# Kernel optimization log

Measured on AMD Instinct MI355X. Metric: run time of the kernel, lower is better.

## Reference

```python
import jax, jax.numpy as jnp
import numpy as np

NUM_PRICAPS, DIM_PRICAPS = 1152, 8
NUM_OBJCAPS, DIM_OBJCAPS = 10, 16
ROUTINGS = 3


def squash(v, axis=-1):
    norm = jnp.linalg.norm(v, axis=axis, keepdims=True)
    scale = norm ** 2 / (1.0 + norm ** 2) / (norm + 1e-8)
    return scale * v


def conv2d(x, w, b, stride):
    out = jax.lax.conv_general_dilated(
        x, w, window_strides=(stride, stride), padding='VALID',
        dimension_numbers=('NCHW', 'OIHW', 'NCHW'))
    return out + b[None, :, None, None]


def setup_inputs() -> dict:
    key = jax.random.key(0)
    ks = jax.random.split(key, 12)
    f32 = jnp.float32
    x = jax.random.uniform(ks[0], (512, 1, 28, 28), dtype=f32)
    conv1_w = jax.random.normal(ks[1], (256, 1, 9, 9), f32) / np.sqrt(1 * 81)
    conv1_b = jnp.zeros((256,), f32)
    conv2_w = jax.random.normal(ks[2], (256, 256, 9, 9), f32) / np.sqrt(256 * 81)
    conv2_b = jnp.zeros((256,), f32)
    route_w = 0.1 * jax.random.normal(ks[3], (NUM_OBJCAPS, NUM_PRICAPS, DIM_OBJCAPS, DIM_PRICAPS), f32)
    d_in = NUM_OBJCAPS * DIM_OBJCAPS  # 160
    dec1_w = jax.random.normal(ks[4], (512, d_in), f32) / np.sqrt(d_in)
    dec1_b = jnp.zeros((512,), f32)
    dec2_w = jax.random.normal(ks[5], (1024, 512), f32) / np.sqrt(512)
    dec2_b = jnp.zeros((1024,), f32)
    dec3_w = jax.random.normal(ks[6], (784, 1024), f32) / np.sqrt(1024)
    dec3_b = jnp.zeros((784,), f32)
    return {'x': x, 'conv1_w': conv1_w, 'conv1_b': conv1_b,
            'conv2_w': conv2_w, 'conv2_b': conv2_b, 'route_w': route_w,
            'dec1_w': dec1_w, 'dec1_b': dec1_b, 'dec2_w': dec2_w,
            'dec2_b': dec2_b, 'dec3_w': dec3_w, 'dec3_b': dec3_b}


def reference(x, conv1_w, conv1_b, conv2_w, conv2_b, route_w,
              dec1_w, dec1_b, dec2_w, dec2_b, dec3_w, dec3_b):
    B = x.shape[0]
    # Encoder: two convs (no activation in original), then capsulate + squash
    h = conv2d(x, conv1_w, conv1_b, 1)            # [B,256,20,20]
    h = conv2d(h, conv2_w, conv2_b, 2)            # [B,256,6,6]
    pricaps = squash(jnp.transpose(h, (0, 2, 3, 1)).reshape(B, NUM_PRICAPS, DIM_PRICAPS))
    # Votes: weight [o,i,k,d] @ incaps [b,i,d] -> [b,o,i,k]
    hat = jnp.einsum('oikd,bid->boik', route_w, pricaps)  # [B,10,1152,16]
    hat_det = jax.lax.stop_gradient(hat)
    b_log = jnp.zeros((B, NUM_OBJCAPS, NUM_PRICAPS), x.dtype)
    c = jax.nn.softmax(jnp.ones((B, NUM_OBJCAPS, NUM_PRICAPS), x.dtype), axis=1)
    outcaps = None
    for i in range(ROUTINGS):
        if i < ROUTINGS - 1:
            outcaps = squash(jnp.sum(c[:, :, :, None] * hat_det, axis=2, keepdims=True))  # [B,10,1,16]
            b_log = b_log + jnp.sum(outcaps * hat_det, axis=-1)
            c = jax.nn.softmax(b_log, axis=1)
        else:
            outcaps = squash(jnp.sum(c[:, :, :, None] * hat, axis=2, keepdims=True))
    objcaps = outcaps[:, :, 0, :]                 # [B,10,16]
    objcaps_len = jnp.linalg.norm(objcaps, axis=-1)  # [B,10]
    # Decoder: reconstruct only the max-length class capsule
    idx_max = jnp.argmax(objcaps_len, axis=1)
    y_onehot = jax.nn.one_hot(idx_max, NUM_OBJCAPS, dtype=objcaps.dtype)
    oc = (objcaps * y_onehot[:, :, None]).reshape(B, -1)  # [B,160]
    d = jax.nn.relu(oc @ dec1_w.T + dec1_b)
    d = jax.nn.relu(d @ dec2_w.T + dec2_b)
    d = jax.nn.sigmoid(d @ dec3_w.T + dec3_b)
    x_recon = jnp.clip(d.reshape(B, 1, 28, 28), 0.0, 1.0)
    return (objcaps_len, x_recon)
```

## Files before the change

### kernel.cpp

```cpp
#include <hip/hip_runtime.h>

typedef short short8 __attribute__((ext_vector_type(8)));
typedef float floatx4 __attribute__((ext_vector_type(4)));

__device__ __forceinline__ unsigned short bf16rn(float x) {
  union { float f; unsigned int u; } v; v.f = x;
  unsigned int r = v.u + 0x7fffu + ((v.u >> 16) & 1u);
  return (unsigned short)(r >> 16);
}
__device__ __forceinline__ float bf16f(unsigned short h) {
  union { unsigned int u; float f; } v; v.u = ((unsigned int)h) << 16;
  return v.f;
}
__device__ __forceinline__ void gload16(const void* g, void* l) {
  __builtin_amdgcn_global_load_lds((const __attribute__((address_space(1))) unsigned int*)g,
                                   (__attribute__((address_space(3))) unsigned int*)l, 16, 0, 0);
}
__device__ __forceinline__ unsigned swz128(int row) {
  return ((row & 1) << 6) | ((row & 2) << 4) | ((row & 4) << 2);
}

__global__ __launch_bounds__(256) void k_w2p(const float* __restrict__ w2,
                                             unsigned short* __restrict__ w2p) {
  __shared__ float sm[20736];
  const int t = threadIdx.x;
  const int co = blockIdx.x;
  for (int q = t; q < 20736; q += 256) sm[q] = w2[(size_t)co * 20736 + q];
  __syncthreads();
  const unsigned s4 = ((co & 1) << 2) | (co & 2) | ((co & 4) >> 2);
  unsigned short* base = w2p + (size_t)co * 64;
  for (int q = t; q < 5184; q += 256) {
    int kk = q >> 6, r = q & 63, cb = r >> 3, cp = r & 7;
    unsigned src = (unsigned)cp ^ s4;
    int half = src >> 2, oct = src & 3;
    const float* col = &sm[(cb * 32 + oct * 8) * 81 + kk];
    union { unsigned short u[8]; uint4 v; } pk;
#pragma unroll
    for (int j = 0; j < 8; ++j) {
      float v = col[j * 81];
      unsigned short hi = bf16rn(v);
      pk.u[j] = half ? bf16rn(v - bf16f(hi)) : hi;
    }
    *(uint4*)(base + (size_t)(kk * 8 + cb) * 16384 + cp * 8) = pk.v;
  }
}

__global__ __launch_bounds__(256) void k_conv1(const float* __restrict__ x, const float* __restrict__ w1,
                                               const float* __restrict__ b1,
                                               unsigned short* __restrict__ h1h,
                                               unsigned short* __restrict__ h1l, int b0) {
  __shared__ float xs[784];
  __shared__ float wsm[64 * 81];
  const int t = threadIdx.x;
  const int b = b0 + blockIdx.x;
  const int coq = blockIdx.y;
  for (int q = t; q < 784; q += 256) xs[q] = x[(size_t)b * 784 + q];
  for (int q = t; q < 5184; q += 256) wsm[q] = w1[coq * 5184 + q];
  __syncthreads();
  const int col = t & 63, yg = t >> 6;
  const int co = coq * 64 + col;
  const float bv = b1[co];
  unsigned short* oh = h1h + (size_t)blockIdx.x * 102400 + co;
  unsigned short* ol = h1l + (size_t)blockIdx.x * 102400 + co;
  for (int yy = 0; yy < 5; ++yy) {
    const int y = yg * 5 + yy;
    float acc[20];
#pragma unroll
    for (int i = 0; i < 20; ++i) acc[i] = bv;
    for (int ky = 0; ky < 9; ++ky) {
      float row[28];
#pragma unroll
      for (int cc = 0; cc < 28; ++cc) row[cc] = xs[(y + ky) * 28 + cc];
#pragma unroll
      for (int kx = 0; kx < 9; ++kx) {
        float wv = wsm[col * 81 + ky * 9 + kx];
#pragma unroll
        for (int xx = 0; xx < 20; ++xx) acc[xx] += row[xx + kx] * wv;
      }
    }
#pragma unroll
    for (int xx = 0; xx < 20; ++xx) {
      unsigned short hi = bf16rn(acc[xx]);
      unsigned short lo = bf16rn(acc[xx] - bf16f(hi));
      size_t p = (size_t)(y * 20 + xx) * 256;
      oh[p] = hi; ol[p] = lo;
    }
  }
}

__global__ __launch_bounds__(256) void k_conv2m(const unsigned short* __restrict__ h1h,
                                                const unsigned short* __restrict__ h1l,
                                                const unsigned short* __restrict__ w2p,
                                                float* __restrict__ part, int b0) {
  __shared__ __align__(16) char smem[40960];
  const int t = threadIdx.x;
  const int lin = blockIdx.x + 144 * blockIdx.z;
  const int xcd = lin & 7, idx = lin >> 3;
  const int zz = xcd & 3;
  const int n0 = ((xcd >> 2) * 72 + idx) * 64;
  const int kk0 = (zz == 0) ? 0 : (21 + 20 * (zz - 1));
  const int kkn = (zz == 0) ? 21 : 20;

  const int wid = t >> 6, lane = t & 63;
  const int l15 = lane & 15, l4 = lane >> 4;
  const int brow = t >> 2, bc4 = t & 3;
  size_t bsrc;
  {
    int nloc = n0 + brow;
    int bi = nloc / 36, pp = nloc - bi * 36;
    int oy = pp / 6, ox = pp - oy * 6;
    bsrc = ((size_t)((bi * 20 + 2 * oy) * 20 + 2 * ox)) * 256;
  }
  const unsigned bswz = swz128(brow);
  const unsigned bo_hi = (unsigned)(brow * 128) + (((unsigned)(bc4 * 16)) ^ bswz);
  const unsigned bo_lo = (unsigned)(brow * 128) + (((unsigned)(64 + bc4 * 16)) ^ bswz);

  floatx4 acc[4][4];
#pragma unroll
  for (int i = 0; i < 4; ++i)
#pragma unroll
    for (int j = 0; j < 4; ++j) acc[i][j] = (floatx4)0.f;

  for (int kq = 0; kq < kkn; ++kq) {
    const int kk = kk0 + kq;
    const int ky = kk / 9, kx = kk - ky * 9;
    const int koff = (ky * 20 + kx) * 256;
    for (int cb = 0; cb < 8; ++cb) {
      const unsigned short* abase = w2p + (size_t)(kk * 8 + cb) * 16384;
#pragma unroll
      for (int j = 0; j < 8; ++j) {
        const int seg = j * 4 + wid;
        gload16(abase + seg * 512 + lane * 8, smem + seg * 1024);
      }
      {
        const unsigned short* sh = h1h + bsrc + koff + cb * 32 + bc4 * 8;
        const unsigned short* sl = h1l + bsrc + koff + cb * 32 + bc4 * 8;
        uint4 vh = *(const uint4*)sh;
        uint4 vl = *(const uint4*)sl;
        *(uint4*)(smem + 32768 + bo_hi) = vh;
        *(uint4*)(smem + 32768 + bo_lo) = vl;
      }
      __syncthreads();
      short8 bh[4], blo[4];
#pragma unroll
      for (int nf = 0; nf < 4; ++nf) {
        const int br = nf * 16 + l15;
        const unsigned s = swz128(br);
        bh[nf] = *(const short8*)(smem + 32768 + br * 128 + (((unsigned)(l4 * 16)) ^ s));
        blo[nf] = *(const short8*)(smem + 32768 + br * 128 + (((unsigned)(64 + l4 * 16)) ^ s));
      }
#pragma unroll
      for (int mf = 0; mf < 4; ++mf) {
        const int ar = wid * 64 + mf * 16 + l15;
        const unsigned s = swz128(ar);
        short8 ah = *(const short8*)(smem + ar * 128 + (((unsigned)(l4 * 16)) ^ s));
        short8 al = *(const short8*)(smem + ar * 128 + (((unsigned)(64 + l4 * 16)) ^ s));
#pragma unroll
        for (int nf = 0; nf < 4; ++nf) {
          acc[mf][nf] = __builtin_amdgcn_mfma_f32_16x16x32_bf16(ah, bh[nf], acc[mf][nf], 0, 0, 0);
          acc[mf][nf] = __builtin_amdgcn_mfma_f32_16x16x32_bf16(ah, blo[nf], acc[mf][nf], 0, 0, 0);
          acc[mf][nf] = __builtin_amdgcn_mfma_f32_16x16x32_bf16(al, bh[nf], acc[mf][nf], 0, 0, 0);
        }
      }
      __syncthreads();
    }
  }
  float* po = part + (size_t)zz * 4718592;
#pragma unroll
  for (int mf = 0; mf < 4; ++mf) {
#pragma unroll
    for (int nf = 0; nf < 4; ++nf) {
      int cog = wid * 64 + mf * 16 + l4 * 4;
      int ng = b0 * 36 + n0 + nf * 16 + l15;
      *(floatx4*)&po[(size_t)ng * 256 + cog] = acc[mf][nf];
    }
  }
}

__global__ __launch_bounds__(256) void k_redsquash(const float* __restrict__ part,
                                                   const float* __restrict__ b2,
                                                   float* __restrict__ pri) {
  const int idx = blockIdx.x * 256 + threadIdx.x;
  const int n = idx >> 5, cap = idx & 31;
  const size_t o = (size_t)n * 256 + cap * 8;
  float s[8];
#pragma unroll
  for (int j = 0; j < 8; ++j) s[j] = b2[cap * 8 + j];
#pragma unroll
  for (int z = 0; z < 4; ++z) {
    const float4 a0 = *(const float4*)&part[(size_t)z * 4718592 + o];
    const float4 a1 = *(const float4*)&part[(size_t)z * 4718592 + o + 4];
    s[0] += a0.x; s[1] += a0.y; s[2] += a0.z; s[3] += a0.w;
    s[4] += a1.x; s[5] += a1.y; s[6] += a1.z; s[7] += a1.w;
  }
  float ss = 0.f;
#pragma unroll
  for (int j = 0; j < 8; ++j) ss += s[j] * s[j];
  float nn = sqrtf(ss);
  float sc = ss / (1.f + ss) / (nn + 1e-8f);
  float4 o0, o1;
  o0.x = s[0] * sc; o0.y = s[1] * sc; o0.z = s[2] * sc; o0.w = s[3] * sc;
  o1.x = s[4] * sc; o1.y = s[5] * sc; o1.z = s[6] * sc; o1.w = s[7] * sc;
  *(float4*)&pri[o] = o0;
  *(float4*)&pri[o + 4] = o1;
}

__global__ __launch_bounds__(256, 2) void k_passA(const float* __restrict__ rw, const float* __restrict__ pri,
                                                  const float* __restrict__ cbuf, float* __restrict__ spart,
                                                  int iter) {
  __shared__ __align__(16) float rw_s[16 * 516];
  __shared__ __align__(16) float p_s[16 * 516];
  __shared__ __align__(16) float c_s[1024];
  const int t = threadIdx.x;
  const int b0 = blockIdx.x * 16, i0 = blockIdx.y * 64, o = blockIdx.z;
  const float* rsrc = rw + (size_t)o * 147456 + (size_t)i0 * 128;
  for (int m = t; m < 2048; m += 256) {
    int il = m >> 5, r = m & 31, d = r >> 1, kh = (m & 1) * 4;
    float4 v = *(const float4*)&rsrc[il * 128 + d * 8 + kh];
    *(float4*)&rw_s[d * 516 + il * 8 + kh] = v;
  }
  for (int m = t; m < 2048; m += 256) {
    int bl = m >> 7, off = (m & 127) * 4;
    float4 v = *(const float4*)&pri[(size_t)(b0 + bl) * 9216 + i0 * 8 + off];
    *(float4*)&p_s[bl * 516 + off] = v;
  }
  if (iter > 0) {
    for (int m = t; m < 256; m += 256) {
      int bl = m >> 4, il4 = (m & 15) * 4;
      float4 v = *(const float4*)&cbuf[(size_t)((b0 + bl) * 10 + o) * 1152 + i0 + il4];
      *(float4*)&c_s[bl * 64 + il4] = v;
    }
  }
  __syncthreads();
  const int d = t & 15, bl = t >> 4;
  float acc = 0.f;
  for (int il = 0; il < 64; ++il) {
    float cv = (iter == 0) ? 0.1f : c_s[bl * 64 + il];
    float4 p0 = *(float4*)&p_s[bl * 516 + il * 8];
    float4 p1 = *(float4*)&p_s[bl * 516 + il * 8 + 4];
    float4 r0 = *(float4*)&rw_s[d * 516 + il * 8];
    float4 r1 = *(float4*)&rw_s[d * 516 + il * 8 + 4];
    float dt = r0.x * p0.x + r0.y * p0.y + r0.z * p0.z + r0.w * p0.w +
               r1.x * p1.x + r1.y * p1.y + r1.z * p1.z + r1.w * p1.w;
    acc += cv * dt;
  }
  spart[((size_t)blockIdx.y * 512 + (b0 + bl)) * 160 + o * 16 + d] = acc;
}

__global__ __launch_bounds__(256) void k_reduce(const float* __restrict__ spart, float* __restrict__ outc,
                                                float* __restrict__ len_out, int final_) {
  const int t = threadIdx.x;
  const int b = blockIdx.x;
  if (t >= 160) return;
  const int o = t / 16, d = t & 15;
  float s = 0.f;
  for (int ic = 0; ic < 18; ++ic) s += spart[((size_t)ic * 512 + b) * 160 + t];
  float ss = s * s;
  ss += __shfl_xor(ss, 1, 16);
  ss += __shfl_xor(ss, 2, 16);
  ss += __shfl_xor(ss, 4, 16);
  ss += __shfl_xor(ss, 8, 16);
  float n = sqrtf(ss);
  float sc = ss / (1.f + ss) / (n + 1e-8f);
  outc[(size_t)b * 160 + t] = sc * s;
  if (final_ && d == 0) len_out[b * 10 + o] = sc * n;
}

__global__ __launch_bounds__(256, 2) void k_passB(const float* __restrict__ rw, const float* __restrict__ pri,
                                                  const float* __restrict__ outc, float* __restrict__ blog,
                                                  int accum) {
  __shared__ __align__(16) float rw_s[16 * 516];
  __shared__ __align__(16) float p_s[16 * 516];
  __shared__ float oc_s[256];
  const int t = threadIdx.x;
  const int b0 = blockIdx.x * 16, i0 = blockIdx.y * 64, o = blockIdx.z;
  const float* rsrc = rw + (size_t)o * 147456 + (size_t)i0 * 128;
  for (int m = t; m < 2048; m += 256) {
    int il = m >> 5, r = m & 31, d = r >> 1, kh = (m & 1) * 4;
    float4 v = *(const float4*)&rsrc[il * 128 + d * 8 + kh];
    *(float4*)&rw_s[d * 516 + il * 8 + kh] = v;
  }
  for (int m = t; m < 2048; m += 256) {
    int bl = m >> 7, off = (m & 127) * 4;
    float4 v = *(const float4*)&pri[(size_t)(b0 + bl) * 9216 + i0 * 8 + off];
    *(float4*)&p_s[bl * 516 + off] = v;
  }
  oc_s[t] = outc[(size_t)(b0 + (t >> 4)) * 160 + o * 16 + (t & 15)];
  __syncthreads();
  const int il0 = t & 15, bl = t >> 4;
  float ocv[16];
#pragma unroll
  for (int k = 0; k < 16; ++k) ocv[k] = oc_s[bl * 16 + k];
#pragma unroll
  for (int is = 0; is < 4; ++is) {
    const int il = is * 16 + il0;
    float4 p0 = *(float4*)&p_s[bl * 516 + il * 8];
    float4 p1 = *(float4*)&p_s[bl * 516 + il * 8 + 4];
    float acc = 0.f;
#pragma unroll
    for (int dd = 0; dd < 16; ++dd) {
      float4 r0 = *(float4*)&rw_s[dd * 516 + il * 8];
      float4 r1 = *(float4*)&rw_s[dd * 516 + il * 8 + 4];
      float h = r0.x * p0.x + r0.y * p0.y + r0.z * p0.z + r0.w * p0.w +
                r1.x * p1.x + r1.y * p1.y + r1.z * p1.z + r1.w * p1.w;
      acc += h * ocv[dd];
    }
    size_t gi = (size_t)((b0 + bl) * 10 + o) * 1152 + i0 + il;
    blog[gi] = accum ? (blog[gi] + acc) : acc;
  }
}

__global__ __launch_bounds__(256) void k_softmax(const float* __restrict__ blog, float* __restrict__ cbuf) {
  const int b = blockIdx.x;
  const int i = blockIdx.y * 256 + threadIdx.x;
  if (i >= 1152) return;
  float v[10];
  float m = -1e30f;
#pragma unroll
  for (int o = 0; o < 10; ++o) {
    v[o] = blog[(size_t)(b * 10 + o) * 1152 + i];
    m = fmaxf(m, v[o]);
  }
  float s = 0.f;
#pragma unroll
  for (int o = 0; o < 10; ++o) {
    v[o] = __expf(v[o] - m);
    s += v[o];
  }
  float inv = 1.f / s;
#pragma unroll
  for (int o = 0; o < 10; ++o) cbuf[(size_t)(b * 10 + o) * 1152 + i] = v[o] * inv;
}

__global__ __launch_bounds__(256) void k_argmax(const float* __restrict__ len_, const float* __restrict__ outc,
                                                int* __restrict__ win, float* __restrict__ oc16) {
  const int b = blockIdx.x * 256 + threadIdx.x;
  if (b >= 512) return;
  float best = len_[b * 10];
  int wi = 0;
  for (int o = 1; o < 10; ++o) {
    float v = len_[b * 10 + o];
    if (v > best) { best = v; wi = o; }
  }
  win[b] = wi;
  for (int k = 0; k < 16; ++k) oc16[b * 16 + k] = outc[(size_t)b * 160 + wi * 16 + k];
}

__global__ __launch_bounds__(256) void k_dec1(const float* __restrict__ oc16, const int* __restrict__ win,
                                              const float* __restrict__ w, const float* __restrict__ bias,
                                              float* __restrict__ d1) {
  const int b = blockIdx.x, t = threadIdx.x;
  const int wi = win[b];
  float ocv[16];
#pragma unroll
  for (int k = 0; k < 16; ++k) ocv[k] = oc16[b * 16 + k];
#pragma unroll
  for (int rep = 0; rep < 2; ++rep) {
    int j = t + rep * 256;
    const float* wr = w + (size_t)j * 160 + wi * 16;
    float acc = bias[j];
#pragma unroll
    for (int k = 0; k < 16; ++k) acc += ocv[k] * wr[k];
    d1[(size_t)b * 512 + j] = fmaxf(acc, 0.f);
  }
}

template <int K, int ACT>
__global__ __launch_bounds__(256) void k_fc(const float* __restrict__ in, const float* __restrict__ w,
                                            const float* __restrict__ bias, float* __restrict__ out, int M) {
  __shared__ __align__(16) float w_s[16 * 64];
  __shared__ __align__(16) float i_s[16 * 64];
  const int t = threadIdx.x;
  const int j0 = blockIdx.x * 64, b0 = blockIdx.y * 64;
  const int tx = t & 15, ty = t >> 4;
  const int jl = tx * 4, bl = ty * 4;
  float acc[4][4];
#pragma unroll
  for (int i = 0; i < 4; ++i)
#pragma unroll
    for (int j = 0; j < 4; ++j) acc[i][j] = 0.f;
  const int rr = t >> 2, kq = (t & 3) * 4;
  for (int k0 = 0; k0 < K; k0 += 16) {
    __syncthreads();
    float4 wv = make_float4(0.f, 0.f, 0.f, 0.f);
    if (j0 + rr < M) wv = *(const float4*)&w[(size_t)(j0 + rr) * K + k0 + kq];
    float4 iv = *(const float4*)&in[(size_t)(b0 + rr) * K + k0 + kq];
    w_s[(kq + 0) * 64 + rr] = wv.x;
    w_s[(kq + 1) * 64 + rr] = wv.y;
    w_s[(kq + 2) * 64 + rr] = wv.z;
    w_s[(kq + 3) * 64 + rr] = wv.w;
    i_s[(kq + 0) * 64 + rr] = iv.x;
    i_s[(kq + 1) * 64 + rr] = iv.y;
    i_s[(kq + 2) * 64 + rr] = iv.z;
    i_s[(kq + 3) * 64 + rr] = iv.w;
    __syncthreads();
#pragma unroll
    for (int k = 0; k < 16; ++k) {
      float4 a = *(float4*)&w_s[k * 64 + jl];
      float4 v = *(float4*)&i_s[k * 64 + bl];
      float av[4] = {a.x, a.y, a.z, a.w};
      float vv[4] = {v.x, v.y, v.z, v.w};
#pragma unroll
      for (int jj = 0; jj < 4; ++jj)
#pragma unroll
        for (int bb = 0; bb < 4; ++bb) acc[jj][bb] += av[jj] * vv[bb];
    }
  }
#pragma unroll
  for (int jj = 0; jj < 4; ++jj) {
    int j = j0 + jl + jj;
    if (j >= M) continue;
    float bs = bias[j];
#pragma unroll
    for (int bb = 0; bb < 4; ++bb) {
      float v = acc[jj][bb] + bs;
      if (ACT == 0) {
        v = fmaxf(v, 0.f);
      } else {
        v = 1.f / (1.f + __expf(-v));
        v = fminf(fmaxf(v, 0.f), 1.f);
      }
      out[(size_t)(b0 + bl + bb) * M + j] = v;
    }
  }
}

extern "C" void kernel_launch(void* const* d_in, const int* in_sizes, int n_in,
                              void* d_out, int out_size, void* d_ws, size_t ws_size,
                              hipStream_t stream) {
  (void)in_sizes; (void)n_in; (void)out_size; (void)ws_size;
  const float* x   = (const float*)d_in[0];
  const float* w1  = (const float*)d_in[1];
  const float* b1  = (const float*)d_in[2];
  const float* w2  = (const float*)d_in[3];
  const float* b2  = (const float*)d_in[4];
  const float* rw  = (const float*)d_in[5];
  const float* d1w = (const float*)d_in[6];
  const float* d1b = (const float*)d_in[7];
  const float* d2w = (const float*)d_in[8];
  const float* d2b = (const float*)d_in[9];
  const float* d3w = (const float*)d_in[10];
  const float* d3b = (const float*)d_in[11];
  float* out = (float*)d_out;

  char* wsb = (char*)d_ws;
  size_t cur = 0;
  auto alloc = [&](size_t bytes) -> char* {
    char* p = wsb + cur;
    cur += (bytes + 255) & ~(size_t)255;
    return p;
  };
  unsigned short* W2P = (unsigned short*)alloc(21233664);
  float* PART = (float*)alloc(75497472);
  float* PRI  = (float*)alloc(18874368);
  float* OUTC = (float*)alloc(327680);
  float* OC   = (float*)alloc(32768);
  int*   WIN  = (int*)alloc(2048);
  float* D1   = (float*)alloc(1048576);
  float* D2   = (float*)alloc(2097152);
  unsigned short* H1H = (unsigned short*)alloc(52428800);
  unsigned short* H1L = (unsigned short*)alloc(52428800);
  float* C  = (float*)H1H;
  float* BL = (float*)((char*)H1H + 23592960);
  float* SP = (float*)((char*)H1H + 47185920);

  k_w2p<<<256, 256, 0, stream>>>(w2, W2P);
  for (int b0 = 0; b0 < 512; b0 += 256) {
    k_conv1<<<dim3(256, 4), 256, 0, stream>>>(x, w1, b1, H1H, H1L, b0);
    k_conv2m<<<dim3(144, 1, 4), 256, 0, stream>>>(H1H, H1L, W2P, PART, b0);
  }
  k_redsquash<<<2304, 256, 0, stream>>>(PART, b2, PRI);

  dim3 gAB(32, 18, 10);
  k_passA<<<gAB, 256, 0, stream>>>(rw, PRI, C, SP, 0);
  k_reduce<<<512, 256, 0, stream>>>(SP, OUTC, out, 0);
  k_passB<<<gAB, 256, 0, stream>>>(rw, PRI, OUTC, BL, 0);
  k_softmax<<<dim3(512, 5), 256, 0, stream>>>(BL, C);
  k_passA<<<gAB, 256, 0, stream>>>(rw, PRI, C, SP, 1);
  k_reduce<<<512, 256, 0, stream>>>(SP, OUTC, out, 0);
  k_passB<<<gAB, 256, 0, stream>>>(rw, PRI, OUTC, BL, 1);
  k_softmax<<<dim3(512, 5), 256, 0, stream>>>(BL, C);
  k_passA<<<gAB, 256, 0, stream>>>(rw, PRI, C, SP, 2);
  k_reduce<<<512, 256, 0, stream>>>(SP, OUTC, out, 1);

  k_argmax<<<2, 256, 0, stream>>>(out, OUTC, WIN, OC);
  k_dec1<<<512, 256, 0, stream>>>(OC, WIN, d1w, d1b, D1);
  k_fc<512, 0><<<dim3(16, 8), 256, 0, stream>>>(D1, d2w, d2b, D2, 1024);
  k_fc<1024, 1><<<dim3(13, 8), 256, 0, stream>>>(D2, d3w, d3b, out + 5120, 784);
}
```

Measured before the change: 1.388 ms.

## Move routing passA onto bf16 MFMA with split-precision prepacked weights

Adds a k_rwp kernel that converts the routing weights once into swizzled hi/lo bf16 tiles stored in the freed PART buffer. passA now folds the coupling coefficients into the primary capsules, splits the product into hi/lo bf16, and computes the weighted sums with 16x16x32 bf16 MFMA using three products (hi*hi, hi*lo, lo*hi) in place of scalar FP32 dot products. The weight tiles are loaded straight into LDS with global_load_lds. This adds a packing kernel and a small precision loss from dropping the lo*lo term, and it reuses PART memory, which assumes PART is no longer needed after redsquash.

```diff
diff --git a/kernel.cpp b/kernel.cpp
--- a/kernel.cpp
+++ b/kernel.cpp
@@ -19,6 +19,9 @@
 __device__ __forceinline__ unsigned swz128(int row) {
   return ((row & 1) << 6) | ((row & 2) << 4) | ((row & 4) << 2);
 }
+__device__ __forceinline__ unsigned s4of(int row) {
+  return ((row & 1) << 2) | (row & 2) | ((row & 4) >> 2);
+}
 
 __global__ __launch_bounds__(256) void k_w2p(const float* __restrict__ w2,
                                              unsigned short* __restrict__ w2p) {
@@ -27,7 +30,7 @@
   const int co = blockIdx.x;
   for (int q = t; q < 20736; q += 256) sm[q] = w2[(size_t)co * 20736 + q];
   __syncthreads();
-  const unsigned s4 = ((co & 1) << 2) | (co & 2) | ((co & 4) >> 2);
+  const unsigned s4 = s4of(co);
   unsigned short* base = w2p + (size_t)co * 64;
   for (int q = t; q < 5184; q += 256) {
     int kk = q >> 6, r = q & 63, cb = r >> 3, cp = r & 7;
@@ -205,46 +208,113 @@
   *(float4*)&pri[o + 4] = o1;
 }
 
-__global__ __launch_bounds__(256, 2) void k_passA(const float* __restrict__ rw, const float* __restrict__ pri,
-                                                  const float* __restrict__ cbuf, float* __restrict__ spart,
-                                                  int iter) {
-  __shared__ __align__(16) float rw_s[16 * 516];
-  __shared__ __align__(16) float p_s[16 * 516];
-  __shared__ __align__(16) float c_s[1024];
-  const int t = threadIdx.x;
-  const int b0 = blockIdx.x * 16, i0 = blockIdx.y * 64, o = blockIdx.z;
-  const float* rsrc = rw + (size_t)o * 147456 + (size_t)i0 * 128;
-  for (int m = t; m < 2048; m += 256) {
-    int il = m >> 5, r = m & 31, d = r >> 1, kh = (m & 1) * 4;
-    float4 v = *(const float4*)&rsrc[il * 128 + d * 8 + kh];
-    *(float4*)&rw_s[d * 516 + il * 8 + kh] = v;
-  }
-  for (int m = t; m < 2048; m += 256) {
-    int bl = m >> 7, off = (m & 127) * 4;
-    float4 v = *(const float4*)&pri[(size_t)(b0 + bl) * 9216 + i0 * 8 + off];
-    *(float4*)&p_s[bl * 516 + off] = v;
-  }
-  if (iter > 0) {
-    for (int m = t; m < 256; m += 256) {
-      int bl = m >> 4, il4 = (m & 15) * 4;
-      float4 v = *(const float4*)&cbuf[(size_t)((b0 + bl) * 10 + o) * 1152 + i0 + il4];
-      *(float4*)&c_s[bl * 64 + il4] = v;
-    }
-  }
-  __syncthreads();
-  const int d = t & 15, bl = t >> 4;
-  float acc = 0.f;
-  for (int il = 0; il < 64; ++il) {
-    float cv = (iter == 0) ? 0.1f : c_s[bl * 64 + il];
-    float4 p0 = *(float4*)&p_s[bl * 516 + il * 8];
-    float4 p1 = *(float4*)&p_s[bl * 516 + il * 8 + 4];
-    float4 r0 = *(float4*)&rw_s[d * 516 + il * 8];
-    float4 r1 = *(float4*)&rw_s[d * 516 + il * 8 + 4];
-    float dt = r0.x * p0.x + r0.y * p0.y + r0.z * p0.z + r0.w * p0.w +
-               r1.x * p1.x + r1.y * p1.y + r1.z * p1.z + r1.w * p1.w;
-    acc += cv * dt;
-  }
-  spart[((size_t)blockIdx.y * 512 + (b0 + bl)) * 160 + o * 16 + d] = acc;
+__global__ __launch_bounds__(256) void k_rwp(const float* __restrict__ rw,
+                                             unsigned short* __restrict__ rwpa) {
+  __shared__ float sm[8192];
+  const int t = threadIdx.x;
+  const int o = blockIdx.x / 18, ic = blockIdx.x % 18;
+  const float* src = rw + (size_t)o * 147456 + (size_t)ic * 8192;
+  for (int q = t; q < 8192; q += 256) sm[q] = src[q];
+  __syncthreads();
+  const int r = t;
+  const int c32 = r >> 4, kobj = r & 15;
+  const unsigned s4 = s4of(r);
+  unsigned short* base = rwpa + (size_t)blockIdx.x * 16384 + r * 64;
+#pragma unroll
+  for (int cp = 0; cp < 8; ++cp) {
+    unsigned c = (unsigned)cp ^ s4;
+    int half = c >> 2;
+    int il = c32 * 4 + (c & 3);
+    const float* col = &sm[il * 128 + kobj * 8];
+    union { unsigned short u[8]; uint4 v; } pk;
+#pragma unroll
+    for (int e = 0; e < 8; ++e) {
+      float v = col[e];
+      unsigned short hi = bf16rn(v);
+      pk.u[e] = half ? bf16rn(v - bf16f(hi)) : hi;
+    }
+    *(uint4*)(base + cp * 8) = pk.v;
+  }
+}
+
+__global__ __launch_bounds__(256, 2) void k_passA(const unsigned short* __restrict__ rwpa,
+                                                  const float* __restrict__ pri,
+                                                  const float* __restrict__ cbuf,
+                                                  float* __restrict__ spart, int iter) {
+  __shared__ __align__(16) char smem[65536];
+  const int t = threadIdx.x;
+  const int b0 = blockIdx.x * 16, ic = blockIdx.y, o = blockIdx.z;
+  const int i0 = ic * 64;
+  {
+    const unsigned short* abase = rwpa + (size_t)(o * 18 + ic) * 16384;
+    const int wid = t >> 6, lane = t & 63;
+#pragma unroll
+    for (int j = 0; j < 8; ++j) {
+      const int seg = j * 4 + wid;
+      gload16(abase + seg * 512 + lane * 8, smem + seg * 1024);
+    }
+  }
+  const int bl = t >> 4, c32 = t & 15;
+  {
+    const float* psrc = pri + (size_t)(b0 + bl) * 9216 + i0 * 8 + c32 * 32;
+    float pv[32];
+#pragma unroll
+    for (int j = 0; j < 8; ++j) {
+      float4 v = *(const float4*)&psrc[j * 4];
+      pv[j * 4 + 0] = v.x; pv[j * 4 + 1] = v.y; pv[j * 4 + 2] = v.z; pv[j * 4 + 3] = v.w;
+    }
+    float cv[4];
+    if (iter == 0) {
+      cv[0] = cv[1] = cv[2] = cv[3] = 0.1f;
+    } else {
+      float4 cc = *(const float4*)&cbuf[(size_t)((b0 + bl) * 10 + o) * 1152 + i0 + c32 * 4];
+      cv[0] = cc.x; cv[1] = cc.y; cv[2] = cc.z; cv[3] = cc.w;
+    }
+    union { unsigned short u[32]; uint4 v[4]; } qh, ql;
+#pragma unroll
+    for (int m = 0; m < 32; ++m) {
+      float q = cv[m >> 3] * pv[m];
+      unsigned short hi = bf16rn(q);
+      qh.u[m] = hi;
+      ql.u[m] = bf16rn(q - bf16f(hi));
+    }
+    const int r = c32 * 16 + bl;
+    const unsigned swz = swz128(r);
+    char* qbase = smem + 32768 + r * 128;
+#pragma unroll
+    for (int j = 0; j < 8; ++j) {
+      int c = (j + c32) & 7;
+      uint4 v = (c < 4) ? qh.v[c & 3] : ql.v[c & 3];
+      *(uint4*)(qbase + (((unsigned)(c * 16)) ^ swz)) = v;
+    }
+  }
+  __syncthreads();
+  const int wid = t >> 6, lane = t & 63;
+  const int l15 = lane & 15, l4 = lane >> 4;
+  floatx4 acc = (floatx4)0.f;
+#pragma unroll
+  for (int cc = 0; cc < 4; ++cc) {
+    const int kc = wid * 4 + cc;
+    const int rr = kc * 16 + l15;
+    const unsigned s = swz128(rr);
+    short8 ah  = *(const short8*)(smem + rr * 128 + (((unsigned)(l4 * 16)) ^ s));
+    short8 al  = *(const short8*)(smem + rr * 128 + (((unsigned)(64 + l4 * 16)) ^ s));
+    short8 bh  = *(const short8*)(smem + 32768 + rr * 128 + (((unsigned)(l4 * 16)) ^ s));
+    short8 blo = *(const short8*)(smem + 32768 + rr * 128 + (((unsigned)(64 + l4 * 16)) ^ s));
+    acc = __builtin_amdgcn_mfma_f32_16x16x32_bf16(ah, bh, acc, 0, 0, 0);
+    acc = __builtin_amdgcn_mfma_f32_16x16x32_bf16(ah, blo, acc, 0, 0, 0);
+    acc = __builtin_amdgcn_mfma_f32_16x16x32_bf16(al, bh, acc, 0, 0, 0);
+  }
+  __syncthreads();
+  *(floatx4*)(smem + wid * 1024 + (l15 * 16 + l4 * 4) * 4) = acc;
+  __syncthreads();
+  {
+    const int obl = t >> 4, okj = t & 15;
+    const float* pp = (const float*)smem;
+    float s = pp[obl * 16 + okj] + pp[256 + obl * 16 + okj] +
+              pp[512 + obl * 16 + okj] + pp[768 + obl * 16 + okj];
+    spart[((size_t)blockIdx.y * 512 + (b0 + obl)) * 160 + o * 16 + okj] = s;
+  }
 }
 
 __global__ __launch_bounds__(256) void k_reduce(const float* __restrict__ spart, float* __restrict__ outc,
@@ -463,6 +533,7 @@
   float* C  = (float*)H1H;
   float* BL = (float*)((char*)H1H + 23592960);
   float* SP = (float*)((char*)H1H + 47185920);
+  unsigned short* RWPA = (unsigned short*)PART;
 
   k_w2p<<<256, 256, 0, stream>>>(w2, W2P);
   for (int b0 = 0; b0 < 512; b0 += 256) {
@@ -470,17 +541,18 @@
     k_conv2m<<<dim3(144, 1, 4), 256, 0, stream>>>(H1H, H1L, W2P, PART, b0);
   }
   k_redsquash<<<2304, 256, 0, stream>>>(PART, b2, PRI);
+  k_rwp<<<180, 256, 0, stream>>>(rw, RWPA);
 
   dim3 gAB(32, 18, 10);
-  k_passA<<<gAB, 256, 0, stream>>>(rw, PRI, C, SP, 0);
+  k_passA<<<gAB, 256, 0, stream>>>(RWPA, PRI, C, SP, 0);
   k_reduce<<<512, 256, 0, stream>>>(SP, OUTC, out, 0);
   k_passB<<<gAB, 256, 0, stream>>>(rw, PRI, OUTC, BL, 0);
   k_softmax<<<dim3(512, 5), 256, 0, stream>>>(BL, C);
-  k_passA<<<gAB, 256, 0, stream>>>(rw, PRI, C, SP, 1);
+  k_passA<<<gAB, 256, 0, stream>>>(RWPA, PRI, C, SP, 1);
   k_reduce<<<512, 256, 0, stream>>>(SP, OUTC, out, 0);
   k_passB<<<gAB, 256, 0, stream>>>(rw, PRI, OUTC, BL, 1);
   k_softmax<<<dim3(512, 5), 256, 0, stream>>>(BL, C);
-  k_passA<<<gAB, 256, 0, stream>>>(rw, PRI, C, SP, 2);
+  k_passA<<<gAB, 256, 0, stream>>>(RWPA, PRI, C, SP, 2);
   k_reduce<<<512, 256, 0, stream>>>(SP, OUTC, out, 1);
 
   k_argmax<<<2, 256, 0, stream>>>(out, OUTC, WIN, OC);
```

Result: no change. 1.414 ms (+1.8%).

## Warp-specialize conv2 MFMA kernel into ping-pong producer/consumer groups with double-buffered LDS

Applied to the files above, without the earlier changes.

k_conv2m now runs 512 threads split into two 256-thread groups over two 40KB LDS buffers. In each K-stage one group runs MFMAs on the current buffer while the other stages the next weight/activation tile, which is meant to hide global-load latency behind compute. Each group keeps its own accumulators, so partial sums go to 8 slices instead of 4. The reduce+squash kernel now runs per half-batch inside the batch loop. In exchange, each block uses 80KB of LDS, which limits blocks per CU, and only half of the waves issue MFMAs at any moment.

```diff
diff --git a/kernel.cpp b/kernel.cpp
--- a/kernel.cpp
+++ b/kernel.cpp
@@ -19,6 +19,9 @@
 __device__ __forceinline__ unsigned swz128(int row) {
   return ((row & 1) << 6) | ((row & 2) << 4) | ((row & 4) << 2);
 }
+__device__ __forceinline__ unsigned s4of(int row) {
+  return ((row & 1) << 2) | (row & 2) | ((row & 4) >> 2);
+}
 
 __global__ __launch_bounds__(256) void k_w2p(const float* __restrict__ w2,
                                              unsigned short* __restrict__ w2p) {
@@ -27,7 +30,7 @@
   const int co = blockIdx.x;
   for (int q = t; q < 20736; q += 256) sm[q] = w2[(size_t)co * 20736 + q];
   __syncthreads();
-  const unsigned s4 = ((co & 1) << 2) | (co & 2) | ((co & 4) >> 2);
+  const unsigned s4 = s4of(co);
   unsigned short* base = w2p + (size_t)co * 64;
   for (int q = t; q < 5184; q += 256) {
     int kk = q >> 6, r = q & 63, cb = r >> 3, cp = r & 7;
@@ -88,12 +91,14 @@
   }
 }
 
-__global__ __launch_bounds__(256) void k_conv2m(const unsigned short* __restrict__ h1h,
-                                                const unsigned short* __restrict__ h1l,
-                                                const unsigned short* __restrict__ w2p,
-                                                float* __restrict__ part, int b0) {
-  __shared__ __align__(16) char smem[40960];
-  const int t = threadIdx.x;
+__global__ __launch_bounds__(512, 4) void k_conv2m(const unsigned short* __restrict__ h1h,
+                                                   const unsigned short* __restrict__ h1l,
+                                                   const unsigned short* __restrict__ w2p,
+                                                   float* __restrict__ part) {
+  __shared__ __align__(16) char smem[81920];
+  const int t = threadIdx.x;
+  const int grp = t >> 8;
+  const int u = t & 255;
   const int lin = blockIdx.x + 144 * blockIdx.z;
   const int xcd = lin & 7, idx = lin >> 3;
   const int zz = xcd & 3;
@@ -101,9 +106,9 @@
   const int kk0 = (zz == 0) ? 0 : (21 + 20 * (zz - 1));
   const int kkn = (zz == 0) ? 21 : 20;
 
-  const int wid = t >> 6, lane = t & 63;
+  const int wid = (t >> 6) & 3, lane = t & 63;
   const int l15 = lane & 15, l4 = lane >> 4;
-  const int brow = t >> 2, bc4 = t & 3;
+  const int brow = u >> 2, bc4 = u & 3;
   size_t bsrc;
   {
     int nloc = n0 + brow;
@@ -121,40 +126,44 @@
 #pragma unroll
     for (int j = 0; j < 4; ++j) acc[i][j] = (floatx4)0.f;
 
-  for (int kq = 0; kq < kkn; ++kq) {
-    const int kk = kk0 + kq;
+  const int S = kkn * 8;
+
+  auto STAGE = [&](int sidx, char* buf) {
+    const int kk = kk0 + (sidx >> 3), cb = sidx & 7;
     const int ky = kk / 9, kx = kk - ky * 9;
-    const int koff = (ky * 20 + kx) * 256;
-    for (int cb = 0; cb < 8; ++cb) {
-      const unsigned short* abase = w2p + (size_t)(kk * 8 + cb) * 16384;
-#pragma unroll
-      for (int j = 0; j < 8; ++j) {
-        const int seg = j * 4 + wid;
-        gload16(abase + seg * 512 + lane * 8, smem + seg * 1024);
-      }
-      {
-        const unsigned short* sh = h1h + bsrc + koff + cb * 32 + bc4 * 8;
-        const unsigned short* sl = h1l + bsrc + koff + cb * 32 + bc4 * 8;
-        uint4 vh = *(const uint4*)sh;
-        uint4 vl = *(const uint4*)sl;
-        *(uint4*)(smem + 32768 + bo_hi) = vh;
-        *(uint4*)(smem + 32768 + bo_lo) = vl;
-      }
-      __syncthreads();
+    const int koff = (ky * 20 + kx) * 256 + cb * 32;
+    const unsigned short* abase = w2p + (size_t)(kk * 8 + cb) * 16384;
+#pragma unroll
+    for (int j = 0; j < 8; ++j) {
+      const int seg = j * 4 + wid;
+      gload16(abase + seg * 512 + lane * 8, buf + seg * 1024);
+    }
+    uint4 vh = *(const uint4*)(h1h + bsrc + koff + bc4 * 8);
+    uint4 vl = *(const uint4*)(h1l + bsrc + koff + bc4 * 8);
+    *(uint4*)(buf + 32768 + bo_hi) = vh;
+    *(uint4*)(buf + 32768 + bo_lo) = vl;
+  };
+
+  if (grp == 1) STAGE(0, smem);
+  __syncthreads();
+
+  for (int s = 0; s < S; ++s) {
+    char* bcur = smem + (s & 1) * 40960;
+    if ((s & 1) == grp) {
       short8 bh[4], blo[4];
 #pragma unroll
       for (int nf = 0; nf < 4; ++nf) {
         const int br = nf * 16 + l15;
-        const unsigned s = swz128(br);
-        bh[nf] = *(const short8*)(smem + 32768 + br * 128 + (((unsigned)(l4 * 16)) ^ s));
-        blo[nf] = *(const short8*)(smem + 32768 + br * 128 + (((unsigned)(64 + l4 * 16)) ^ s));
+        const unsigned sw = swz128(br);
+        bh[nf]  = *(const short8*)(bcur + 32768 + br * 128 + (((unsigned)(l4 * 16)) ^ sw));
+        blo[nf] = *(const short8*)(bcur + 32768 + br * 128 + (((unsigned)(64 + l4 * 16)) ^ sw));
       }
 #pragma unroll
       for (int mf = 0; mf < 4; ++mf) {
         const int ar = wid * 64 + mf * 16 + l15;
-        const unsigned s = swz128(ar);
-        short8 ah = *(const short8*)(smem + ar * 128 + (((unsigned)(l4 * 16)) ^ s));
-        short8 al = *(const short8*)(smem + ar * 128 + (((unsigned)(64 + l4 * 16)) ^ s));
+        const unsigned sw = swz128(ar);
+        short8 ah = *(const short8*)(bcur + ar * 128 + (((unsigned)(l4 * 16)) ^ sw));
+        short8 al = *(const short8*)(bcur + ar * 128 + (((unsigned)(64 + l4 * 16)) ^ sw));
 #pragma unroll
         for (int nf = 0; nf < 4; ++nf) {
           acc[mf][nf] = __builtin_amdgcn_mfma_f32_16x16x32_bf16(ah, bh[nf], acc[mf][nf], 0, 0, 0);
@@ -162,16 +171,18 @@
           acc[mf][nf] = __builtin_amdgcn_mfma_f32_16x16x32_bf16(al, bh[nf], acc[mf][nf], 0, 0, 0);
         }
       }
-      __syncthreads();
-    }
-  }
-  float* po = part + (size_t)zz * 4718592;
+    } else if (s + 1 < S) {
+      STAGE(s + 1, smem + ((s + 1) & 1) * 40960);
+    }
+    __syncthreads();
+  }
+  float* po = part + (size_t)(zz * 2 + grp) * 2359296;
 #pragma unroll
   for (int mf = 0; mf < 4; ++mf) {
 #pragma unroll
     for (int nf = 0; nf < 4; ++nf) {
       int cog = wid * 64 + mf * 16 + l4 * 4;
-      int ng = b0 * 36 + n0 + nf * 16 + l15;
+      int ng = n0 + nf * 16 + l15;
       *(floatx4*)&po[(size_t)ng * 256 + cog] = acc[mf][nf];
     }
   }
@@ -187,9 +198,9 @@
 #pragma unroll
   for (int j = 0; j < 8; ++j) s[j] = b2[cap * 8 + j];
 #pragma unroll
-  for (int z = 0; z < 4; ++z) {
-    const float4 a0 = *(const float4*)&part[(size_t)z * 4718592 + o];
-    const float4 a1 = *(const float4*)&part[(size_t)z * 4718592 + o + 4];
+  for (int z = 0; z < 8; ++z) {
+    const float4 a0 = *(const float4*)&part[(size_t)z * 2359296 + o];
+    const float4 a1 = *(const float4*)&part[(size_t)z * 2359296 + o + 4];
     s[0] += a0.x; s[1] += a0.y; s[2] += a0.z; s[3] += a0.w;
     s[4] += a1.x; s[5] += a1.y; s[6] += a1.z; s[7] += a1.w;
   }
@@ -467,9 +478,9 @@
   k_w2p<<<256, 256, 0, stream>>>(w2, W2P);
   for (int b0 = 0; b0 < 512; b0 += 256) {
     k_conv1<<<dim3(256, 4), 256, 0, stream>>>(x, w1, b1, H1H, H1L, b0);
-    k_conv2m<<<dim3(144, 1, 4), 256, 0, stream>>>(H1H, H1L, W2P, PART, b0);
-  }
-  k_redsquash<<<2304, 256, 0, stream>>>(PART, b2, PRI);
+    k_conv2m<<<dim3(144, 1, 4), 512, 0, stream>>>(H1H, H1L, W2P, PART);
+    k_redsquash<<<1152, 256, 0, stream>>>(PART, b2, PRI + (size_t)b0 * 36 * 256);
+  }
 
   dim3 gAB(32, 18, 10);
   k_passA<<<gAB, 256, 0, stream>>>(rw, PRI, C, SP, 0);
```

New measurement: 2.418 ms. 1.74x slower.
